# Kernel optimization log

Measured on AMD Instinct MI355X. Metric: run time of the kernel, lower is better.

## Reference

```python
import jax, jax.numpy as jnp
import numpy as np

N = 50000      # nodes
E = 800000     # edges
F_NODE = 64    # num_node_features
F_EDGE = 16    # num_edge_features
C = 64         # out_channels
L = 3          # n_hidden_layers
G = 512        # num graphs in batch
NCLS = 10      # num_classes
EPS = 1e-5


def _lin_init(k, shape, fan_in):
    lim = 1.0 / np.sqrt(fan_in)
    return jax.random.uniform(k, shape, jnp.float32, -lim, lim)


def setup_inputs() -> dict:
    key = jax.random.key(0)
    ks = jax.random.split(key, 32)
    inp = {
        "x": jax.random.normal(ks[0], (N, F_NODE), jnp.float32),
        "edge_index": jax.random.randint(ks[1], (2, E), 0, N, jnp.int32),
        "batch": ((jnp.arange(N) * G) // N).astype(jnp.int32),  # sorted, covers all graphs
        "dropout": 0,
        "edge_attr": jax.random.uniform(ks[2], (E, F_EDGE), jnp.float32),
        # conv1: PDNConv(F_NODE, C, F_EDGE, F_EDGE). torch Linear layout [out,in].
        "c1_lw": _lin_init(ks[3], (C, F_NODE), F_NODE),
        "c1_w1": _lin_init(ks[4], (F_EDGE, F_EDGE), F_EDGE),
        "c1_b1": _lin_init(ks[5], (F_EDGE,), F_EDGE),
        "c1_w2": _lin_init(ks[6], (1, F_EDGE), F_EDGE),
        "c1_b2": _lin_init(ks[7], (1,), F_EDGE),
        # hidden_conv_1 / hidden_conv_2: L stacked PDNConv(C, C, F_EDGE, F_EDGE)
        "h1_lw": _lin_init(ks[8], (L, C, C), C),
        "h1_w1": _lin_init(ks[9], (L, F_EDGE, F_EDGE), F_EDGE),
        "h1_b1": _lin_init(ks[10], (L, F_EDGE), F_EDGE),
        "h1_w2": _lin_init(ks[11], (L, 1, F_EDGE), F_EDGE),
        "h1_b2": _lin_init(ks[12], (L, 1), F_EDGE),
        "h2_lw": _lin_init(ks[13], (L, C, C), C),
        "h2_w1": _lin_init(ks[14], (L, F_EDGE, F_EDGE), F_EDGE),
        "h2_b1": _lin_init(ks[15], (L, F_EDGE), F_EDGE),
        "h2_w2": _lin_init(ks[16], (L, 1, F_EDGE), F_EDGE),
        "h2_b2": _lin_init(ks[17], (L, 1), F_EDGE),
        # final classifier Linear(C, NCLS)
        "lin_w": _lin_init(ks[18], (NCLS, C), C),
        "lin_b": _lin_init(ks[19], (NCLS,), C),
    }
    return inp


def _pdn_conv(x, row, col, loop, edge_attr, lw, w1, b1, w2, b2):
    """PDNConv: edge-MLP weight -> add self loops -> gcn_norm -> gather-scale-scatter."""
    # edge weight MLP: Linear -> ReLU -> Linear -> Sigmoid, squeeze to [E]
    w = jax.nn.sigmoid(jnp.squeeze(jax.nn.relu(edge_attr @ w1.T + b1) @ w2.T + b2, -1))
    wf = jnp.concatenate([w, jnp.ones((x.shape[0],), x.dtype)])  # self-loop weight 1
    r = jnp.concatenate([row, loop])
    c = jnp.concatenate([col, loop])
    deg = jax.ops.segment_sum(wf, c, num_segments=x.shape[0])
    dis = jnp.where(deg > 0, 1.0 / jnp.sqrt(deg), 0.0)
    norm = dis[r] * wf * dis[c]                 # gcn_norm edge coefficients
    xl = x @ lw.T                                # node transform [N, C]
    msg = xl[r] * norm[:, None]                  # gather + scale [E+N, C]
    return jax.ops.segment_sum(msg, c, num_segments=x.shape[0])


def _batch_norm(x):
    # fresh BatchNorm each forward: weight=1, bias=0, training-mode batch stats
    mu = jnp.mean(x, axis=0)
    var = jnp.mean(jnp.square(x - mu), axis=0)  # biased var
    return (x - mu) * jax.lax.rsqrt(var + EPS)


def reference(x, edge_index, batch, dropout, edge_attr,
              c1_lw, c1_w1, c1_b1, c1_w2, c1_b2,
              h1_lw, h1_w1, h1_b1, h1_w2, h1_b2,
              h2_lw, h2_w1, h2_b1, h2_w2, h2_b2,
              lin_w, lin_b):
    row, col = edge_index[0], edge_index[1]
    loop = jnp.arange(x.shape[0], dtype=row.dtype)

    x = _pdn_conv(x, row, col, loop, edge_attr, c1_lw, c1_w1, c1_b1, c1_w2, c1_b2)
    x0 = x
    for i in range(L):
        x = jax.nn.relu(_batch_norm(x))
        x = _pdn_conv(x, row, col, loop, edge_attr,
                      h1_lw[i], h1_w1[i], h1_b1[i], h1_w2[i], h1_b2[i])
    x1 = x + x0
    x = x + x0
    for i in range(L):
        x = jax.nn.relu(_batch_norm(x))
        x = _pdn_conv(x, row, col, loop, edge_attr,
                      h2_lw[i], h2_w1[i], h2_b1[i], h2_w2[i], h2_b2[i])
    x2 = jax.nn.relu(x + x0 + x1)
    pooled = jax.ops.segment_max(x2, batch, num_segments=G)  # global max pool [G, C]
    # dropout p passed in is 0 / eval -> identity
    return pooled @ lin_w.T + lin_b
```

## Files before the change

### kernel.cpp

```cpp
#include <hip/hip_runtime.h>
#include <hip/hip_bf16.h>
#include <hip/hip_fp16.h>
#include <math.h>

#define NN 50000
#define NE 800000
#define FE 16
#define CC 64
#define NG 512
#define NCLS 10
#define NCONV 7
#define SCAN_B 49

typedef float v2f __attribute__((ext_vector_type(2)));

struct MlpP { const float* w1; const float* b1; const float* w2; const float* b2; };
struct MlpAll { MlpP p[NCONV]; };

__device__ __forceinline__ float4 ld_half4(const __half* p) {
  uint2 r = *reinterpret_cast<const uint2*>(p);
  __half2 a = *reinterpret_cast<const __half2*>(&r.x);
  __half2 b = *reinterpret_cast<const __half2*>(&r.y);
  float2 fa = __half22float2(a);
  float2 fb = __half22float2(b);
  return make_float4(fa.x, fa.y, fb.x, fb.y);
}

__global__ __launch_bounds__(256) void k_hist(const int* __restrict__ ecol, int* __restrict__ cnt) {
  int e = blockIdx.x * 256 + threadIdx.x;
  if (e < NE) atomicAdd(&cnt[ecol[e]], 1);
}

__global__ __launch_bounds__(1024) void k_scanA(const int* __restrict__ cnt, int* __restrict__ excl,
                                                int* __restrict__ bsum) {
  __shared__ int sc[1024];
  int t = threadIdx.x;
  int i = blockIdx.x * 1024 + t;
  int v = (i < NN) ? cnt[i] : 0;
  sc[t] = v;
  __syncthreads();
  for (int off = 1; off < 1024; off <<= 1) {
    int u = (t >= off) ? sc[t - off] : 0;
    __syncthreads();
    sc[t] += u;
    __syncthreads();
  }
  if (i < NN) excl[i] = sc[t] - v;
  if (t == 1023) bsum[blockIdx.x] = sc[1023];
}

__global__ void k_scanB(const int* __restrict__ bsum, int* __restrict__ boff) {
  int lane = threadIdx.x;
  int v = (lane < SCAN_B) ? bsum[lane] : 0;
  int own = v;
  for (int off = 1; off < 64; off <<= 1) {
    int u = __shfl_up(v, off);
    if (lane >= off) v += u;
  }
  if (lane < SCAN_B) boff[lane] = v - own;
}

__global__ __launch_bounds__(1024) void k_scanC(const int* __restrict__ excl, const int* __restrict__ boff,
                                                int* __restrict__ cptr, int* __restrict__ cursor) {
  int i = blockIdx.x * 1024 + threadIdx.x;
  if (i < NN) {
    int p = excl[i] + boff[blockIdx.x];
    cptr[i] = p;
    cursor[i] = p;
  }
  if (i == 0) cptr[NN] = NE;
}

__global__ __launch_bounds__(256) void k_scatter(
    const int* __restrict__ erow, const int* __restrict__ ecol,
    int* __restrict__ cursor, int* __restrict__ csrc, int* __restrict__ pos) {
  int e = blockIdx.x * 256 + threadIdx.x;
  if (e >= NE) return;
  int c = ecol[e];
  int p = atomicAdd(&cursor[c], 1);
  csrc[p] = erow[e];
  pos[e] = p;
}

__global__ __launch_bounds__(256) void k_mlp(
    const int* __restrict__ pos, const float* __restrict__ ea,
    float* __restrict__ wcsr8, MlpAll mw) {
  int ep = blockIdx.x * 256 + threadIdx.x;
  if (ep >= NE / 4) return;
  int e0 = ep * 4;
  const float4* ea4 = reinterpret_cast<const float4*>(ea + (size_t)e0 * 16);
  float4 A0 = ea4[0],  A1 = ea4[1],  A2 = ea4[2],  A3 = ea4[3];
  float4 B0 = ea4[4],  B1 = ea4[5],  B2 = ea4[6],  B3 = ea4[7];
  float4 C0 = ea4[8],  C1 = ea4[9],  C2 = ea4[10], C3 = ea4[11];
  float4 D0 = ea4[12], D1 = ea4[13], D2 = ea4[14], D3 = ea4[15];
  v2f aA[16], aB[16];
  aA[0]  = (v2f){A0.x, B0.x}; aA[1]  = (v2f){A0.y, B0.y}; aA[2]  = (v2f){A0.z, B0.z}; aA[3]  = (v2f){A0.w, B0.w};
  aA[4]  = (v2f){A1.x, B1.x}; aA[5]  = (v2f){A1.y, B1.y}; aA[6]  = (v2f){A1.z, B1.z}; aA[7]  = (v2f){A1.w, B1.w};
  aA[8]  = (v2f){A2.x, B2.x}; aA[9]  = (v2f){A2.y, B2.y}; aA[10] = (v2f){A2.z, B2.z}; aA[11] = (v2f){A2.w, B2.w};
  aA[12] = (v2f){A3.x, B3.x}; aA[13] = (v2f){A3.y, B3.y}; aA[14] = (v2f){A3.z, B3.z}; aA[15] = (v2f){A3.w, B3.w};
  aB[0]  = (v2f){C0.x, D0.x}; aB[1]  = (v2f){C0.y, D0.y}; aB[2]  = (v2f){C0.z, D0.z}; aB[3]  = (v2f){C0.w, D0.w};
  aB[4]  = (v2f){C1.x, D1.x}; aB[5]  = (v2f){C1.y, D1.y}; aB[6]  = (v2f){C1.z, D1.z}; aB[7]  = (v2f){C1.w, D1.w};
  aB[8]  = (v2f){C2.x, D2.x}; aB[9]  = (v2f){C2.y, D2.y}; aB[10] = (v2f){C2.z, D2.z}; aB[11] = (v2f){C2.w, D2.w};
  aB[12] = (v2f){C3.x, D3.x}; aB[13] = (v2f){C3.y, D3.y}; aB[14] = (v2f){C3.z, D3.z}; aB[15] = (v2f){C3.w, D3.w};
  int4 pp = *reinterpret_cast<const int4*>(pos + e0);
  float wv0[NCONV], wv1[NCONV], wv2[NCONV], wv3[NCONV];
  #pragma unroll
  for (int j = 0; j < NCONV; ++j) {
    const float* w1 = mw.p[j].w1;
    const float* b1 = mw.p[j].b1;
    const float* w2 = mw.p[j].w2;
    float b2v = mw.p[j].b2[0];
    v2f zA = {b2v, b2v}, zB = {b2v, b2v};
    #pragma unroll
    for (int k = 0; k < 16; ++k) {
      float bk = b1[k];
      float wk = w2[k];
      v2f hA = {bk, bk}, hB = {bk, bk};
      #pragma unroll
      for (int m = 0; m < 16; ++m) {
        float wm = w1[k * 16 + m];
        hA += aA[m] * wm;
        hB += aB[m] * wm;
      }
      hA.x = hA.x > 0.f ? hA.x : 0.f;
      hA.y = hA.y > 0.f ? hA.y : 0.f;
      hB.x = hB.x > 0.f ? hB.x : 0.f;
      hB.y = hB.y > 0.f ? hB.y : 0.f;
      zA += hA * wk;
      zB += hB * wk;
    }
    wv0[j] = 1.f / (1.f + __expf(-zA.x));
    wv1[j] = 1.f / (1.f + __expf(-zA.y));
    wv2[j] = 1.f / (1.f + __expf(-zB.x));
    wv3[j] = 1.f / (1.f + __expf(-zB.y));
  }
  float4* d0 = reinterpret_cast<float4*>(wcsr8 + (size_t)pp.x * 8);
  d0[0] = make_float4(wv0[0], wv0[1], wv0[2], wv0[3]);
  d0[1] = make_float4(wv0[4], wv0[5], wv0[6], 0.f);
  float4* d1 = reinterpret_cast<float4*>(wcsr8 + (size_t)pp.y * 8);
  d1[0] = make_float4(wv1[0], wv1[1], wv1[2], wv1[3]);
  d1[1] = make_float4(wv1[4], wv1[5], wv1[6], 0.f);
  float4* d2 = reinterpret_cast<float4*>(wcsr8 + (size_t)pp.z * 8);
  d2[0] = make_float4(wv2[0], wv2[1], wv2[2], wv2[3]);
  d2[1] = make_float4(wv2[4], wv2[5], wv2[6], 0.f);
  float4* d3 = reinterpret_cast<float4*>(wcsr8 + (size_t)pp.w * 8);
  d3[0] = make_float4(wv3[0], wv3[1], wv3[2], wv3[3]);
  d3[1] = make_float4(wv3[4], wv3[5], wv3[6], 0.f);
}

__global__ __launch_bounds__(256) void k_repack(const float* __restrict__ wcsr8, float* __restrict__ wpl) {
  int p = blockIdx.x * 256 + threadIdx.x;
  if (p >= NE) return;
  const float4* q = reinterpret_cast<const float4*>(wcsr8 + (size_t)p * 8);
  float4 a = q[0], b = q[1];
  wpl[0 * (size_t)NE + p] = a.x;
  wpl[1 * (size_t)NE + p] = a.y;
  wpl[2 * (size_t)NE + p] = a.z;
  wpl[3 * (size_t)NE + p] = a.w;
  wpl[4 * (size_t)NE + p] = b.x;
  wpl[5 * (size_t)NE + p] = b.y;
  wpl[6 * (size_t)NE + p] = b.z;
}

__global__ __launch_bounds__(256) void k_deg(const float* __restrict__ wcsr8,
                                             const int* __restrict__ cptr,
                                             float* __restrict__ dis) {
  int n = blockIdx.x * 256 + threadIdx.x;
  if (n >= NN) return;
  int lo = cptr[n], hi = cptr[n + 1];
  float s0=0,s1=0,s2=0,s3=0,s4=0,s5=0,s6=0;
  for (int k = lo; k < hi; ++k) {
    const float4* q = reinterpret_cast<const float4*>(wcsr8 + (size_t)k * 8);
    float4 a = q[0], b = q[1];
    s0+=a.x; s1+=a.y; s2+=a.z; s3+=a.w; s4+=b.x; s5+=b.y; s6+=b.z;
  }
  dis[0*NN+n]=rsqrtf(s0+1.f); dis[1*NN+n]=rsqrtf(s1+1.f); dis[2*NN+n]=rsqrtf(s2+1.f);
  dis[3*NN+n]=rsqrtf(s3+1.f); dis[4*NN+n]=rsqrtf(s4+1.f); dis[5*NN+n]=rsqrtf(s5+1.f);
  dis[6*NN+n]=rsqrtf(s6+1.f);
}

__global__ __launch_bounds__(256) void k_lwt(const float* __restrict__ c1, const float* __restrict__ h1,
                                             const float* __restrict__ h2, float* __restrict__ lwT) {
  int id = blockIdx.x * 256 + threadIdx.x;
  if (id >= NCONV * CC * CC) return;
  int j = id >> 12;
  int r = id & 4095;
  int co = r >> 6, ci = r & 63;
  const float* src = (j == 0) ? c1 : (j <= 3 ? h1 + (j - 1) * 4096 : h2 + (j - 4) * 4096);
  lwT[j * 4096 + ci * 64 + co] = src[co * 64 + ci];
}

__global__ __launch_bounds__(256) void k_bnstat(const float* __restrict__ src, float* __restrict__ accum) {
  __shared__ float sS[256], sQ[256];
  int t = threadIdx.x;
  int c = t & 63, rg = t >> 6;
  int base = blockIdx.x * 196;
  float S = 0.f, Q = 0.f;
  for (int rr = rg; rr < 196; rr += 4) {
    int r = base + rr;
    if (r < NN) { float v = src[r * 64 + c]; S += v; Q += v * v; }
  }
  sS[t] = S; sQ[t] = Q;
  __syncthreads();
  if (t < 128) { sS[t] += sS[t + 128]; sQ[t] += sQ[t + 128]; }
  __syncthreads();
  if (t < 64) {
    atomicAdd(&accum[c], sS[t] + sS[t + 64]);
    atomicAdd(&accum[64 + c], sQ[t] + sQ[t + 64]);
  }
}

__global__ __launch_bounds__(256) void k_gemm(const float* __restrict__ src, const float* __restrict__ lwT,
                                              const float* __restrict__ accum, const float* __restrict__ dis,
                                              __half* __restrict__ dstH, int useBN) {
  __shared__ float xs[64 * 65];
  int t = threadIdx.x;
  int rows0 = blockIdx.x * 64;
  for (int i = 0; i < 4; ++i) {
    int f = t + i * 256;
    int r = f >> 4, c4 = (f & 15) * 4;
    int row = rows0 + r;
    float4 v = make_float4(0.f, 0.f, 0.f, 0.f);
    if (row < NN) v = *reinterpret_cast<const float4*>(src + (size_t)row * 64 + c4);
    if (useBN) {
      float4 S = *reinterpret_cast<const float4*>(accum + c4);
      float4 Q = *reinterpret_cast<const float4*>(accum + 64 + c4);
      float mu, var, rs;
      mu = S.x * (1.0f/NN); var = Q.x*(1.0f/NN)-mu*mu; var = var<0.f?0.f:var; rs = rsqrtf(var+1e-5f);
      v.x = (v.x-mu)*rs; v.x = v.x>0.f?v.x:0.f;
      mu = S.y * (1.0f/NN); var = Q.y*(1.0f/NN)-mu*mu; var = var<0.f?0.f:var; rs = rsqrtf(var+1e-5f);
      v.y = (v.y-mu)*rs; v.y = v.y>0.f?v.y:0.f;
      mu = S.z * (1.0f/NN); var = Q.z*(1.0f/NN)-mu*mu; var = var<0.f?0.f:var; rs = rsqrtf(var+1e-5f);
      v.z = (v.z-mu)*rs; v.z = v.z>0.f?v.z:0.f;
      mu = S.w * (1.0f/NN); var = Q.w*(1.0f/NN)-mu*mu; var = var<0.f?0.f:var; rs = rsqrtf(var+1e-5f);
      v.w = (v.w-mu)*rs; v.w = v.w>0.f?v.w:0.f;
    }
    xs[r * 65 + c4 + 0] = v.x;
    xs[r * 65 + c4 + 1] = v.y;
    xs[r * 65 + c4 + 2] = v.z;
    xs[r * 65 + c4 + 3] = v.w;
  }
  __syncthreads();
  int lane = t & 63;
  int cobase = __builtin_amdgcn_readfirstlane((t >> 6) << 4);
  float acc[16];
  #pragma unroll
  for (int u = 0; u < 16; ++u) acc[u] = 0.f;
  #pragma unroll 8
  for (int ci = 0; ci < 64; ++ci) {
    float xv = xs[lane * 65 + ci];
    const float* wrow = lwT + ci * 64 + cobase;
    #pragma unroll
    for (int u = 0; u < 16; ++u) acc[u] += xv * wrow[u];
  }
  __syncthreads();
  int row = rows0 + lane;
  float d = (row < NN) ? dis[row] : 0.f;
  #pragma unroll
  for (int u = 0; u < 16; ++u) xs[lane * 65 + cobase + u] = acc[u] * d;
  __syncthreads();
  for (int i = 0; i < 4; ++i) {
    int f = t + i * 256;
    int r = f >> 4, c4 = (f & 15) * 4;
    int orow = rows0 + r;
    if (orow < NN) {
      __half2 h0 = __floats2half2_rn(xs[r*65+c4+0], xs[r*65+c4+1]);
      __half2 h1 = __floats2half2_rn(xs[r*65+c4+2], xs[r*65+c4+3]);
      uint2 pk;
      pk.x = *reinterpret_cast<unsigned int*>(&h0);
      pk.y = *reinterpret_cast<unsigned int*>(&h1);
      *reinterpret_cast<uint2*>(dstH + (size_t)orow * 64 + c4) = pk;
    }
  }
}

__global__ __launch_bounds__(256) void k_agg(const __half* __restrict__ T, const float* __restrict__ wj,
                                             const int* __restrict__ csrc, const int* __restrict__ cptr,
                                             const float* __restrict__ dis, float* __restrict__ out,
                                             const float* __restrict__ skipA, const float* __restrict__ skipX1,
                                             float* __restrict__ outX1, const int* __restrict__ batch,
                                             int* __restrict__ poolI, int wstride, int mode) {
  int t = threadIdx.x;
  int n = blockIdx.x * 4 + (t >> 6);
  if (n >= NN) return;
  int lane = t & 63;
  int e4 = lane >> 4;
  int cq = lane & 15;
  int lo = cptr[n], hi = cptr[n + 1];

  float4 tn = ld_half4(T + (size_t)n * 64 + cq * 4);
  float4 acc;
  acc.x = e4 == 0 ? tn.x : 0.f;
  acc.y = e4 == 0 ? tn.y : 0.f;
  acc.z = e4 == 0 ? tn.z : 0.f;
  acc.w = e4 == 0 ? tn.w : 0.f;

  int base = lo;
  int ka = base + e4;
  int kb = base + 4 + e4;
  bool va = ka < hi, vb = kb < hi;
  int   sa = va ? csrc[ka] : n;
  float wa = va ? wj[(size_t)ka * wstride] : 0.f;
  int   sb = vb ? csrc[kb] : n;
  float wb = vb ? wj[(size_t)kb * wstride] : 0.f;
  while (base < hi) {
    int csa = sa, csb = sb;
    float cwa = wa, cwb = wb;
    base += 8;
    ka = base + e4;
    kb = base + 4 + e4;
    va = ka < hi; vb = kb < hi;
    sa = va ? csrc[ka] : n;
    wa = va ? wj[(size_t)ka * wstride] : 0.f;
    sb = vb ? csrc[kb] : n;
    wb = vb ? wj[(size_t)kb * wstride] : 0.f;
    float4 qa = ld_half4(T + (size_t)csa * 64 + cq * 4);
    float4 qb = ld_half4(T + (size_t)csb * 64 + cq * 4);
    acc.x += cwa * qa.x + cwb * qb.x;
    acc.y += cwa * qa.y + cwb * qb.y;
    acc.z += cwa * qa.z + cwb * qb.z;
    acc.w += cwa * qa.w + cwb * qb.w;
  }

  acc.x += __shfl_xor(acc.x, 16); acc.y += __shfl_xor(acc.y, 16);
  acc.z += __shfl_xor(acc.z, 16); acc.w += __shfl_xor(acc.w, 16);
  acc.x += __shfl_xor(acc.x, 32); acc.y += __shfl_xor(acc.y, 32);
  acc.z += __shfl_xor(acc.z, 32); acc.w += __shfl_xor(acc.w, 32);

  if (e4 != 0) return;
  float d = dis[n];
  float4 v = make_float4(acc.x * d, acc.y * d, acc.z * d, acc.w * d);
  size_t ridx = (size_t)n * 16 + cq;
  if (mode == 1) {
    float4 a = reinterpret_cast<const float4*>(skipA)[ridx];
    float4 sv = make_float4(v.x + a.x, v.y + a.y, v.z + a.z, v.w + a.w);
    reinterpret_cast<float4*>(outX1)[ridx] = sv;
  } else if (mode == 2) {
    float4 a = reinterpret_cast<const float4*>(skipA)[ridx];
    float4 x1 = reinterpret_cast<const float4*>(skipX1)[ridx];
    float4 sv = make_float4(v.x + a.x + x1.x, v.y + a.y + x1.y, v.z + a.z + x1.z, v.w + a.w + x1.w);
    sv.x = sv.x > 0.f ? sv.x : 0.f;
    sv.y = sv.y > 0.f ? sv.y : 0.f;
    sv.z = sv.z > 0.f ? sv.z : 0.f;
    sv.w = sv.w > 0.f ? sv.w : 0.f;
    int g = batch[n];
    int* pb = poolI + (size_t)g * 64 + cq * 4;
    atomicMax(pb + 0, __float_as_int(sv.x));
    atomicMax(pb + 1, __float_as_int(sv.y));
    atomicMax(pb + 2, __float_as_int(sv.z));
    atomicMax(pb + 3, __float_as_int(sv.w));
  } else {
    reinterpret_cast<float4*>(out)[ridx] = v;
  }
}

__global__ __launch_bounds__(256) void k_cls(const float* __restrict__ pooled, const float* __restrict__ lw,
                                             const float* __restrict__ lb, float* __restrict__ out) {
  int id = blockIdx.x * 256 + threadIdx.x;
  if (id >= NG * NCLS) return;
  int g = id / NCLS, k = id % NCLS;
  float acc = lb[k];
  #pragma unroll 8
  for (int c = 0; c < 64; ++c) acc += pooled[g * 64 + c] * lw[k * 64 + c];
  out[id] = acc;
}

extern "C" void kernel_launch(void* const* d_in, const int* in_sizes, int n_in,
                              void* d_out, int out_size, void* d_ws, size_t ws_size,
                              hipStream_t stream) {
  (void)in_sizes; (void)n_in; (void)out_size;
  const float* x     = (const float*)d_in[0];
  const int*   ei    = (const int*)d_in[1];
  const int*   batch = (const int*)d_in[2];
  const float* ea    = (const float*)d_in[4];
  const float* c1_lw = (const float*)d_in[5];
  const float* c1_w1 = (const float*)d_in[6];
  const float* c1_b1 = (const float*)d_in[7];
  const float* c1_w2 = (const float*)d_in[8];
  const float* c1_b2 = (const float*)d_in[9];
  const float* h1_lw = (const float*)d_in[10];
  const float* h1_w1 = (const float*)d_in[11];
  const float* h1_b1 = (const float*)d_in[12];
  const float* h1_w2 = (const float*)d_in[13];
  const float* h1_b2 = (const float*)d_in[14];
  const float* h2_lw = (const float*)d_in[15];
  const float* h2_w1 = (const float*)d_in[16];
  const float* h2_b1 = (const float*)d_in[17];
  const float* h2_w2 = (const float*)d_in[18];
  const float* h2_b2 = (const float*)d_in[19];
  const float* lin_w = (const float*)d_in[20];
  const float* lin_b = (const float*)d_in[21];
  float* out = (float*)d_out;

  char* base = (char*)d_ws;
  size_t off = 0;
  auto alloc = [&](size_t bytes) -> size_t {
    size_t o = off;
    off = (off + bytes + 255) & ~(size_t)255;
    return o;
  };
  size_t o_wcsr8  = alloc((size_t)NE * 8 * 4);
  size_t o_csrc   = alloc((size_t)NE * 4);
  size_t o_pos    = alloc((size_t)NE * 4);
  size_t o_cptr   = alloc((size_t)(NN + 1) * 4);
  size_t o_excl   = alloc((size_t)NN * 4);
  size_t o_bsum   = alloc((size_t)64 * 4);
  size_t o_boff   = alloc((size_t)64 * 4);
  size_t o_cnt    = alloc((size_t)NN * 4);
  size_t o_accum  = alloc((size_t)6 * 128 * 4);
  size_t o_dis    = alloc((size_t)NCONV * NN * 4);
  size_t o_lwt    = alloc((size_t)NCONV * 4096 * 4);
  size_t o_T      = alloc((size_t)NN * 64 * 2);
  size_t o_A      = alloc((size_t)NN * 64 * 4);
  size_t o_B      = alloc((size_t)NN * 64 * 4);
  size_t o_X1     = alloc((size_t)NN * 64 * 4);
  size_t o_pool   = alloc((size_t)NG * 64 * 4);
  size_t o_wpl    = alloc((size_t)NCONV * NE * 4);
  bool use_planes = (off <= ws_size);

  float* wcsr8  = (float*)(base + o_wcsr8);
  int*   csrc   = (int*)(base + o_csrc);
  int*   pos    = (int*)(base + o_pos);
  int*   cptr   = (int*)(base + o_cptr);
  int*   excl   = (int*)(base + o_excl);
  int*   bsum   = (int*)(base + o_bsum);
  int*   boff   = (int*)(base + o_boff);
  int*   cnt    = (int*)(base + o_cnt);
  float* accum  = (float*)(base + o_accum);
  float* dis    = (float*)(base + o_dis);
  float* lwt    = (float*)(base + o_lwt);
  __half* T     = (__half*)(base + o_T);
  float* A      = (float*)(base + o_A);
  float* B      = (float*)(base + o_B);
  float* X1     = (float*)(base + o_X1);
  float* pooled = (float*)(base + o_pool);
  float* wpl    = (float*)(base + o_wpl);

  hipMemsetAsync(base + o_cnt, 0, o_dis - o_cnt, stream);
  hipMemsetAsync(base + o_pool, 0, (size_t)NG * 64 * 4, stream);

  const int* erow = ei;
  const int* ecol = ei + NE;

  k_hist<<<(NE + 255) / 256, 256, 0, stream>>>(ecol, cnt);
  k_scanA<<<SCAN_B, 1024, 0, stream>>>(cnt, excl, bsum);
  k_scanB<<<1, 64, 0, stream>>>(bsum, boff);
  k_scanC<<<SCAN_B, 1024, 0, stream>>>(excl, boff, cptr, cnt);
  k_scatter<<<(NE + 255) / 256, 256, 0, stream>>>(erow, ecol, cnt, csrc, pos);

  MlpAll mw;
  mw.p[0] = {c1_w1, c1_b1, c1_w2, c1_b2};
  for (int i = 0; i < 3; ++i) {
    mw.p[1 + i] = {h1_w1 + i * 256, h1_b1 + i * 16, h1_w2 + i * 16, h1_b2 + i};
    mw.p[4 + i] = {h2_w1 + i * 256, h2_b1 + i * 16, h2_w2 + i * 16, h2_b2 + i};
  }
  k_mlp<<<(NE / 4 + 255) / 256, 256, 0, stream>>>(pos, ea, wcsr8, mw);
  if (use_planes) k_repack<<<(NE + 255) / 256, 256, 0, stream>>>(wcsr8, wpl);
  k_deg<<<(NN + 255) / 256, 256, 0, stream>>>(wcsr8, cptr, dis);
  k_lwt<<<(NCONV * 4096) / 256, 256, 0, stream>>>(c1_lw, h1_lw, h2_lw, lwt);

  const int GB = (NN + 63) / 64;
  const int AB = (NN + 3) / 4;
  auto wbase = [&](int j) -> const float* {
    return use_planes ? (wpl + (size_t)j * NE) : (wcsr8 + j);
  };
  const int WS = use_planes ? 1 : 8;

  k_gemm<<<GB, 256, 0, stream>>>(x, lwt, nullptr, dis, T, 0);
  k_agg<<<AB, 256, 0, stream>>>(T, wbase(0), csrc, cptr, dis, A,
                                nullptr, nullptr, nullptr, nullptr, nullptr, WS, 0);

  for (int i = 0; i < 3; ++i) {
    const float* src = (i == 0) ? A : B;
    k_bnstat<<<256, 256, 0, stream>>>(src, accum + i * 128);
    k_gemm<<<GB, 256, 0, stream>>>(src, lwt + (1 + i) * 4096, accum + i * 128,
                                   dis + (size_t)(1 + i) * NN, T, 1);
    int mode = (i == 2) ? 1 : 0;
    k_agg<<<AB, 256, 0, stream>>>(T, wbase(1 + i), csrc, cptr,
                                  dis + (size_t)(1 + i) * NN, B, A, nullptr, X1,
                                  nullptr, nullptr, WS, mode);
  }
  for (int i = 0; i < 3; ++i) {
    const float* src = (i == 0) ? X1 : B;
    k_bnstat<<<256, 256, 0, stream>>>(src, accum + (3 + i) * 128);
    k_gemm<<<GB, 256, 0, stream>>>(src, lwt + (4 + i) * 4096, accum + (3 + i) * 128,
                                   dis + (size_t)(4 + i) * NN, T, 1);
    int mode = (i == 2) ? 2 : 0;
    k_agg<<<AB, 256, 0, stream>>>(T, wbase(4 + i), csrc, cptr,
                                  dis + (size_t)(4 + i) * NN, B, A, X1, nullptr,
                                  batch, (int*)pooled, WS, mode);
  }

  k_cls<<<(NG * NCLS + 255) / 256, 256, 0, stream>>>(pooled, lin_w, lin_b, out);
}
```

Measured before the change: 599.0 us.

## Store intermediate node activations A, B, X1 in fp16 and coalesce agg writes

The intermediate node-feature buffers (A, B, X1) move from fp32 to fp16. BN stats, the GEMM input loads and the skip-connection reads become half-precision loads, which halves their memory traffic. The aggregation kernel now stages each block's four output rows in shared memory and writes them with a single coalesced 64-lane store, at the cost of an extra __syncthreads. The grid assumes NN is divisible by 4, and fp16 storage adds rounding to the residual and BN paths.

```diff
diff --git a/kernel.cpp b/kernel.cpp
--- a/kernel.cpp
+++ b/kernel.cpp
@@ -24,6 +24,15 @@
   float2 fa = __half22float2(a);
   float2 fb = __half22float2(b);
   return make_float4(fa.x, fa.y, fb.x, fb.y);
+}
+
+__device__ __forceinline__ uint2 pk_half4(float4 v) {
+  __half2 h0 = __floats2half2_rn(v.x, v.y);
+  __half2 h1 = __floats2half2_rn(v.z, v.w);
+  uint2 pk;
+  pk.x = *reinterpret_cast<unsigned int*>(&h0);
+  pk.y = *reinterpret_cast<unsigned int*>(&h1);
+  return pk;
 }
 
 __global__ __launch_bounds__(256) void k_hist(const int* __restrict__ ecol, int* __restrict__ cnt) {
@@ -190,7 +199,7 @@
   lwT[j * 4096 + ci * 64 + co] = src[co * 64 + ci];
 }
 
-__global__ __launch_bounds__(256) void k_bnstat(const float* __restrict__ src, float* __restrict__ accum) {
+__global__ __launch_bounds__(256) void k_bnstat(const __half* __restrict__ src, float* __restrict__ accum) {
   __shared__ float sS[256], sQ[256];
   int t = threadIdx.x;
   int c = t & 63, rg = t >> 6;
@@ -198,7 +207,10 @@
   float S = 0.f, Q = 0.f;
   for (int rr = rg; rr < 196; rr += 4) {
     int r = base + rr;
-    if (r < NN) { float v = src[r * 64 + c]; S += v; Q += v * v; }
+    if (r < NN) {
+      float v = __half2float(src[(size_t)r * 64 + c]);
+      S += v; Q += v * v;
+    }
   }
   sS[t] = S; sQ[t] = Q;
   __syncthreads();
@@ -210,7 +222,8 @@
   }
 }
 
-__global__ __launch_bounds__(256) void k_gemm(const float* __restrict__ src, const float* __restrict__ lwT,
+__global__ __launch_bounds__(256) void k_gemm(const float* __restrict__ srcF, const __half* __restrict__ srcH,
+                                              const float* __restrict__ lwT,
                                               const float* __restrict__ accum, const float* __restrict__ dis,
                                               __half* __restrict__ dstH, int useBN) {
   __shared__ float xs[64 * 65];
@@ -221,7 +234,10 @@
     int r = f >> 4, c4 = (f & 15) * 4;
     int row = rows0 + r;
     float4 v = make_float4(0.f, 0.f, 0.f, 0.f);
-    if (row < NN) v = *reinterpret_cast<const float4*>(src + (size_t)row * 64 + c4);
+    if (row < NN) {
+      if (srcF) v = *reinterpret_cast<const float4*>(srcF + (size_t)row * 64 + c4);
+      else      v = ld_half4(srcH + (size_t)row * 64 + c4);
+    }
     if (useBN) {
       float4 S = *reinterpret_cast<const float4*>(accum + c4);
       float4 Q = *reinterpret_cast<const float4*>(accum + 64 + c4);
@@ -264,25 +280,22 @@
     int r = f >> 4, c4 = (f & 15) * 4;
     int orow = rows0 + r;
     if (orow < NN) {
-      __half2 h0 = __floats2half2_rn(xs[r*65+c4+0], xs[r*65+c4+1]);
-      __half2 h1 = __floats2half2_rn(xs[r*65+c4+2], xs[r*65+c4+3]);
-      uint2 pk;
-      pk.x = *reinterpret_cast<unsigned int*>(&h0);
-      pk.y = *reinterpret_cast<unsigned int*>(&h1);
-      *reinterpret_cast<uint2*>(dstH + (size_t)orow * 64 + c4) = pk;
+      float4 v = make_float4(xs[r*65+c4], xs[r*65+c4+1], xs[r*65+c4+2], xs[r*65+c4+3]);
+      *reinterpret_cast<uint2*>(dstH + (size_t)orow * 64 + c4) = pk_half4(v);
     }
   }
 }
 
 __global__ __launch_bounds__(256) void k_agg(const __half* __restrict__ T, const float* __restrict__ wj,
                                              const int* __restrict__ csrc, const int* __restrict__ cptr,
-                                             const float* __restrict__ dis, float* __restrict__ out,
-                                             const float* __restrict__ skipA, const float* __restrict__ skipX1,
-                                             float* __restrict__ outX1, const int* __restrict__ batch,
-                                             int* __restrict__ poolI, int wstride, int mode) {
+                                             const float* __restrict__ dis, __half* __restrict__ dst,
+                                             const __half* __restrict__ skipA, const __half* __restrict__ skipX1,
+                                             const int* __restrict__ batch, int* __restrict__ poolI,
+                                             int wstride, int mode) {
+  __shared__ uint2 smu[64];
   int t = threadIdx.x;
-  int n = blockIdx.x * 4 + (t >> 6);
-  if (n >= NN) return;
+  int wv = t >> 6;
+  int n = blockIdx.x * 4 + wv;
   int lane = t & 63;
   int e4 = lane >> 4;
   int cq = lane & 15;
@@ -327,30 +340,37 @@
   acc.x += __shfl_xor(acc.x, 32); acc.y += __shfl_xor(acc.y, 32);
   acc.z += __shfl_xor(acc.z, 32); acc.w += __shfl_xor(acc.w, 32);
 
-  if (e4 != 0) return;
-  float d = dis[n];
-  float4 v = make_float4(acc.x * d, acc.y * d, acc.z * d, acc.w * d);
-  size_t ridx = (size_t)n * 16 + cq;
-  if (mode == 1) {
-    float4 a = reinterpret_cast<const float4*>(skipA)[ridx];
-    float4 sv = make_float4(v.x + a.x, v.y + a.y, v.z + a.z, v.w + a.w);
-    reinterpret_cast<float4*>(outX1)[ridx] = sv;
-  } else if (mode == 2) {
-    float4 a = reinterpret_cast<const float4*>(skipA)[ridx];
-    float4 x1 = reinterpret_cast<const float4*>(skipX1)[ridx];
-    float4 sv = make_float4(v.x + a.x + x1.x, v.y + a.y + x1.y, v.z + a.z + x1.z, v.w + a.w + x1.w);
-    sv.x = sv.x > 0.f ? sv.x : 0.f;
-    sv.y = sv.y > 0.f ? sv.y : 0.f;
-    sv.z = sv.z > 0.f ? sv.z : 0.f;
-    sv.w = sv.w > 0.f ? sv.w : 0.f;
-    int g = batch[n];
-    int* pb = poolI + (size_t)g * 64 + cq * 4;
-    atomicMax(pb + 0, __float_as_int(sv.x));
-    atomicMax(pb + 1, __float_as_int(sv.y));
-    atomicMax(pb + 2, __float_as_int(sv.z));
-    atomicMax(pb + 3, __float_as_int(sv.w));
-  } else {
-    reinterpret_cast<float4*>(out)[ridx] = v;
+  if (e4 == 0) {
+    float d = dis[n];
+    float4 v = make_float4(acc.x * d, acc.y * d, acc.z * d, acc.w * d);
+    if (mode == 1) {
+      float4 a = ld_half4(skipA + (size_t)n * 64 + cq * 4);
+      v.x += a.x; v.y += a.y; v.z += a.z; v.w += a.w;
+      smu[wv * 16 + cq] = pk_half4(v);
+    } else if (mode == 2) {
+      float4 a = ld_half4(skipA + (size_t)n * 64 + cq * 4);
+      float4 x1 = ld_half4(skipX1 + (size_t)n * 64 + cq * 4);
+      float4 sv = make_float4(v.x + a.x + x1.x, v.y + a.y + x1.y, v.z + a.z + x1.z, v.w + a.w + x1.w);
+      sv.x = sv.x > 0.f ? sv.x : 0.f;
+      sv.y = sv.y > 0.f ? sv.y : 0.f;
+      sv.z = sv.z > 0.f ? sv.z : 0.f;
+      sv.w = sv.w > 0.f ? sv.w : 0.f;
+      int g = batch[n];
+      int* pb = poolI + (size_t)g * 64 + cq * 4;
+      atomicMax(pb + 0, __float_as_int(sv.x));
+      atomicMax(pb + 1, __float_as_int(sv.y));
+      atomicMax(pb + 2, __float_as_int(sv.z));
+      atomicMax(pb + 3, __float_as_int(sv.w));
+    } else {
+      smu[wv * 16 + cq] = pk_half4(v);
+    }
+  }
+  if (mode != 2) {
+    __syncthreads();
+    if (t < 64) {
+      int n0 = blockIdx.x * 4;
+      reinterpret_cast<uint2*>(dst + (size_t)n0 * 64)[t] = smu[t];
+    }
   }
 }
 
@@ -411,9 +431,9 @@
   size_t o_dis    = alloc((size_t)NCONV * NN * 4);
   size_t o_lwt    = alloc((size_t)NCONV * 4096 * 4);
   size_t o_T      = alloc((size_t)NN * 64 * 2);
-  size_t o_A      = alloc((size_t)NN * 64 * 4);
-  size_t o_B      = alloc((size_t)NN * 64 * 4);
-  size_t o_X1     = alloc((size_t)NN * 64 * 4);
+  size_t o_A      = alloc((size_t)NN * 64 * 2);
+  size_t o_B      = alloc((size_t)NN * 64 * 2);
+  size_t o_X1     = alloc((size_t)NN * 64 * 2);
   size_t o_pool   = alloc((size_t)NG * 64 * 4);
   size_t o_wpl    = alloc((size_t)NCONV * NE * 4);
   bool use_planes = (off <= ws_size);
@@ -430,9 +450,9 @@
   float* dis    = (float*)(base + o_dis);
   float* lwt    = (float*)(base + o_lwt);
   __half* T     = (__half*)(base + o_T);
-  float* A      = (float*)(base + o_A);
-  float* B      = (float*)(base + o_B);
-  float* X1     = (float*)(base + o_X1);
+  __half* A     = (__half*)(base + o_A);
+  __half* B     = (__half*)(base + o_B);
+  __half* X1    = (__half*)(base + o_X1);
   float* pooled = (float*)(base + o_pool);
   float* wpl    = (float*)(base + o_wpl);
 
@@ -460,34 +480,35 @@
   k_lwt<<<(NCONV * 4096) / 256, 256, 0, stream>>>(c1_lw, h1_lw, h2_lw, lwt);
 
   const int GB = (NN + 63) / 64;
-  const int AB = (NN + 3) / 4;
+  const int AB = NN / 4;
   auto wbase = [&](int j) -> const float* {
     return use_planes ? (wpl + (size_t)j * NE) : (wcsr8 + j);
   };
   const int WS = use_planes ? 1 : 8;
 
-  k_gemm<<<GB, 256, 0, stream>>>(x, lwt, nullptr, dis, T, 0);
+  k_gemm<<<GB, 256, 0, stream>>>(x, nullptr, lwt, nullptr, dis, T, 0);
   k_agg<<<AB, 256, 0, stream>>>(T, wbase(0), csrc, cptr, dis, A,
-                                nullptr, nullptr, nullptr, nullptr, nullptr, WS, 0);
+                                nullptr, nullptr, nullptr, nullptr, WS, 0);
 
   for (int i = 0; i < 3; ++i) {
-    const float* src = (i == 0) ? A : B;
+    const __half* src = (i == 0) ? A : B;
     k_bnstat<<<256, 256, 0, stream>>>(src, accum + i * 128);
-    k_gemm<<<GB, 256, 0, stream>>>(src, lwt + (1 + i) * 4096, accum + i * 128,
+    k_gemm<<<GB, 256, 0, stream>>>(nullptr, src, lwt + (1 + i) * 4096, accum + i * 128,
                                    dis + (size_t)(1 + i) * NN, T, 1);
     int mode = (i == 2) ? 1 : 0;
+    __half* dst = (i == 2) ? X1 : B;
     k_agg<<<AB, 256, 0, stream>>>(T, wbase(1 + i), csrc, cptr,
-                                  dis + (size_t)(1 + i) * NN, B, A, nullptr, X1,
+                                  dis + (size_t)(1 + i) * NN, dst, A, nullptr,
                                   nullptr, nullptr, WS, mode);
   }
   for (int i = 0; i < 3; ++i) {
-    const float* src = (i == 0) ? X1 : B;
+    const __half* src = (i == 0) ? X1 : B;
     k_bnstat<<<256, 256, 0, stream>>>(src, accum + (3 + i) * 128);
-    k_gemm<<<GB, 256, 0, stream>>>(src, lwt + (4 + i) * 4096, accum + (3 + i) * 128,
+    k_gemm<<<GB, 256, 0, stream>>>(nullptr, src, lwt + (4 + i) * 4096, accum + (3 + i) * 128,
                                    dis + (size_t)(4 + i) * NN, T, 1);
     int mode = (i == 2) ? 2 : 0;
     k_agg<<<AB, 256, 0, stream>>>(T, wbase(4 + i), csrc, cptr,
-                                  dis + (size_t)(4 + i) * NN, B, A, X1, nullptr,
+                                  dis + (size_t)(4 + i) * NN, B, A, X1,
                                   batch, (int*)pooled, WS, mode);
   }
 
```

New measurement: 609.8 us. About the same (+1.8%).
